# Performance work log

Measured on AMD Instinct MI355X. Metric: run time of the kernel, lower is better.

## Reference

```python
import jax, jax.numpy as jnp
import numpy as np

N = 100000          # total nodes
E = 1200000         # total edges
IN_CH = 22          # NUM_NODES_SINGLE_TEAM * 2
HID = 64
NUM_CLASSES = 3
G = 256             # graphs in batch


def setup_inputs() -> dict:
    key = jax.random.key(0)
    ks = jax.random.split(key, 12)
    x = jax.random.normal(ks[0], (N, IN_CH), jnp.float32)
    edge_index = jax.random.randint(ks[1], (2, E), 0, N, dtype=jnp.int32)
    edge_weight = jax.random.uniform(ks[2], (E,), jnp.float32)
    batch = jnp.sort(jax.random.randint(ks[3], (N,), 0, G, dtype=jnp.int32))

    def lin_w(k, fi, fo):
        return jax.random.normal(k, (fi, fo), jnp.float32) / np.float32(np.sqrt(fi))

    return {
        "x": x,
        "edge_index": edge_index,
        "edge_weight": edge_weight,
        "batch": batch,
        "W1": lin_w(ks[4], IN_CH, HID),  "b1": jnp.zeros((HID,), jnp.float32),
        "W2": lin_w(ks[5], HID, HID),    "b2": jnp.zeros((HID,), jnp.float32),
        "fw1": lin_w(ks[6], HID, HID),   "fb1": jnp.zeros((HID,), jnp.float32),
        "fw2": lin_w(ks[7], HID, NUM_CLASSES), "fb2": jnp.zeros((NUM_CLASSES,), jnp.float32),
    }


def gcn_conv(x, edge_index, edge_weight, W, b):
    """PyG GCNConv: self-loops (weight 1) + symmetric normalization + scatter-add."""
    n = x.shape[0]
    loop = jnp.arange(n, dtype=edge_index.dtype)
    row = jnp.concatenate([edge_index[0], loop])
    col = jnp.concatenate([edge_index[1], loop])
    w = jnp.concatenate([edge_weight, jnp.ones((n,), x.dtype)])
    deg = jax.ops.segment_sum(w, col, num_segments=n)        # weighted in-degree
    safe = jnp.where(deg > 0, deg, 1.0)
    dinv = jnp.where(deg > 0, jax.lax.rsqrt(safe), 0.0)
    norm = dinv[row] * w * dinv[col]                         # [E+N]
    h = x @ W                                                # transform first (d small)
    msg = norm[:, None] * h[row]                             # gather + scale
    out = jax.ops.segment_sum(msg, col, num_segments=n)      # scatter-add
    return out + b


def reference(x, edge_index, edge_weight, batch, W1, b1, W2, b2, fw1, fb1, fw2, fb2):
    h = jax.nn.relu(gcn_conv(x, edge_index, edge_weight, W1, b1))
    h = jax.nn.relu(gcn_conv(h, edge_index, edge_weight, W2, b2))
    # global_mean_pool
    sums = jax.ops.segment_sum(h, batch, num_segments=G)
    cnt = jax.ops.segment_sum(jnp.ones((h.shape[0],), h.dtype), batch, num_segments=G)
    pooled = sums / jnp.maximum(cnt, 1.0)[:, None]
    h = jax.nn.relu(pooled @ fw1 + fb1)
    return h @ fw2 + fb2
```

## Files before the change

### kernel.cpp

```cpp
#include <hip/hip_runtime.h>
#include <hip/hip_bf16.h>
#include <hip/hip_fp16.h>


#define HIDC 64
#define MTILE 128
#define XS_STRIDE (MTILE + 4)
#define BSHIFT 9
#define SPAN 512
#define NBKT_MAX 256
#define BCHUNK 2048

typedef unsigned long long u64;

__global__ void k_zero_int(int* p, int n) {
    int i = blockIdx.x * blockDim.x + threadIdx.x;
    if (i < n) p[i] = 0;
}

__global__ __launch_bounds__(256) void k_bin_count(const int* __restrict__ col,
                                                   int* bucket_cnt, int E, int NB) {
    __shared__ int hist[NBKT_MAX];
    int tid = threadIdx.x;
    for (int i = tid; i < NB; i += 256) hist[i] = 0;
    __syncthreads();
    int base = blockIdx.x * 8192;
    for (int j = 0; j < 32; ++j) {
        int e = base + j * 256 + tid;
        if (e < E) atomicAdd(&hist[col[e] >> BSHIFT], 1);
    }
    __syncthreads();
    for (int i = tid; i < NB; i += 256)
        if (hist[i]) atomicAdd(&bucket_cnt[i], hist[i]);
}

__global__ void k_bucket_scan(const int* __restrict__ bucket_cnt, int* __restrict__ bucket_base,
                              int* __restrict__ cursor_g, int NB, int E) {
    __shared__ int s[256];
    int t = threadIdx.x;
    int v = (t < NB) ? bucket_cnt[t] : 0;
    s[t] = v;
    __syncthreads();
    for (int o = 1; o < 256; o <<= 1) {
        int x = (t >= o) ? s[t - o] : 0;
        __syncthreads();
        s[t] += x;
        __syncthreads();
    }
    if (t < NB) { int ex = s[t] - v; bucket_base[t] = ex; cursor_g[t] = ex; }
    if (t == 0) bucket_base[NB] = E;
}

__global__ __launch_bounds__(256) void k_bin_scatter(const int* __restrict__ row,
                                                     const int* __restrict__ col,
                                                     const float* __restrict__ ew,
                                                     int* cursor_g, u64* __restrict__ bedges,
                                                     int E, int NB) {
    __shared__ int hist[NBKT_MAX], binoff[NBKT_MAX], cursor[NBKT_MAX], gbase[NBKT_MAX];
    __shared__ int s[256];
    __shared__ u64 stage[BCHUNK];
    __shared__ unsigned char binid[BCHUNK];
    int tid = threadIdx.x;
    for (int i = tid; i < NB; i += 256) hist[i] = 0;
    __syncthreads();
    int base = blockIdx.x * BCHUNK;
    u64 pk[8]; int bb[8];
#pragma unroll
    for (int j = 0; j < 8; ++j) {
        int e = base + j * 256 + tid;
        if (e < E) {
            int c = col[e];
            bb[j] = c >> BSHIFT;
            pk[j] = ((u64)__float_as_uint(ew[e]) << 32) |
                    ((u64)(unsigned)row[e] << BSHIFT) | (unsigned)(c & (SPAN - 1));
            atomicAdd(&hist[bb[j]], 1);
        } else bb[j] = -1;
    }
    __syncthreads();
    {
        int v = (tid < NB) ? hist[tid] : 0;
        s[tid] = v;
        __syncthreads();
        for (int o = 1; o < 256; o <<= 1) {
            int x = (tid >= o) ? s[tid - o] : 0;
            __syncthreads();
            s[tid] += x;
            __syncthreads();
        }
        if (tid < NB) { binoff[tid] = s[tid] - v; cursor[tid] = s[tid] - v; }
    }
    __syncthreads();
#pragma unroll
    for (int j = 0; j < 8; ++j)
        if (bb[j] >= 0) {
            int pos = atomicAdd(&cursor[bb[j]], 1);
            stage[pos] = pk[j];
            binid[pos] = (unsigned char)bb[j];
        }
    __syncthreads();
    if (tid < NB && hist[tid] > 0) gbase[tid] = atomicAdd(&cursor_g[tid], hist[tid]);
    __syncthreads();
    int total = min(BCHUNK, E - base);
    for (int i = tid; i < total; i += 256) {
        int b = binid[i];
        bedges[(size_t)gbase[b] + (i - binoff[b])] = stage[i];
    }
}

__global__ __launch_bounds__(256) void k_bucket_process(const u64* __restrict__ bedges,
                                                        const int* __restrict__ bucket_base,
                                                        u64* __restrict__ csr,
                                                        float* __restrict__ dinv,
                                                        int* __restrict__ off,
                                                        int N, int E, int NB) {
    __shared__ float deg[SPAN];
    __shared__ int cL[SPAN];
    __shared__ int offL[SPAN];
    __shared__ int s[256];
    int b = blockIdx.x, tid = threadIdx.x;
    int ebase = bucket_base[b], ecnt = bucket_base[b + 1] - ebase;
    int nd0 = b << BSHIFT;
    int ndn = min(SPAN, N - nd0);
    for (int i = tid; i < SPAN; i += 256) { deg[i] = 1.0f; cL[i] = 0; }
    __syncthreads();
    for (int e = tid; e < ecnt; e += 256) {
        u64 p = bedges[ebase + e];
        int colin = (int)(p & (SPAN - 1));
        atomicAdd(&deg[colin], __uint_as_float((unsigned)(p >> 32)));
        atomicAdd(&cL[colin], 1);
    }
    __syncthreads();
    int p0 = cL[2 * tid], p1 = cL[2 * tid + 1];
    s[tid] = p0 + p1;
    __syncthreads();
    for (int o = 1; o < 256; o <<= 1) {
        int x = (tid >= o) ? s[tid - o] : 0;
        __syncthreads();
        s[tid] += x;
        __syncthreads();
    }
    int ex = s[tid] - (p0 + p1);
    offL[2 * tid] = ex;
    offL[2 * tid + 1] = ex + p0;
    __syncthreads();
    for (int i = tid; i < ndn; i += 256) {
        dinv[nd0 + i] = rsqrtf(deg[i]);
        off[nd0 + i] = ebase + offL[i];
    }
    for (int i = tid; i < SPAN; i += 256) cL[i] = offL[i];
    if (b == NB - 1 && tid == 0) off[N] = E;
    __syncthreads();
    for (int e = tid; e < ecnt; e += 256) {
        u64 p = bedges[ebase + e];
        int colin = (int)(p & (SPAN - 1));
        int src = (int)((p >> BSHIFT) & 0x7FFFFF);
        int slot = atomicAdd(&cL[colin], 1);
        csr[(size_t)ebase + slot] = ((u64)(unsigned)src << 32) | (unsigned)(p >> 32);
    }
}

template <int K>
__global__ __launch_bounds__(256) void k_gemm_tile(const float* __restrict__ x,
                                                   const float* __restrict__ W,
                                                   const float* __restrict__ dinv,
                                                   __half* __restrict__ h, int n) {
    __shared__ float xs[K * XS_STRIDE];
    __shared__ float ws[K * HIDC];
    int tid = threadIdx.x;
    int n0 = blockIdx.x * MTILE;

    for (int i = tid; i < K * HIDC; i += 256) ws[i] = W[i];

    if constexpr ((K & 3) == 0) {
        constexpr int KQ = K / 4;
        for (int i = tid; i < MTILE * KQ; i += 256) {
            int r = i / KQ, kq = i - r * KQ;
            float4 v = make_float4(0.f, 0.f, 0.f, 0.f);
            if (n0 + r < n)
                v = *reinterpret_cast<const float4*>(x + (size_t)(n0 + r) * K + kq * 4);
            int k0 = kq * 4;
            xs[(k0 + 0) * XS_STRIDE + r] = v.x;
            xs[(k0 + 1) * XS_STRIDE + r] = v.y;
            xs[(k0 + 2) * XS_STRIDE + r] = v.z;
            xs[(k0 + 3) * XS_STRIDE + r] = v.w;
        }
    } else {
        for (int i = tid; i < MTILE * K; i += 256) {
            int r = i / K, k = i - r * K;
            float v = (n0 + r < n) ? x[(size_t)(n0 + r) * K + k] : 0.f;
            xs[k * XS_STRIDE + r] = v;
        }
    }
    __syncthreads();

    int c0 = (tid & 15) * 4;
    int m0 = (tid >> 4) * 8;
    float acc[8][4];
#pragma unroll
    for (int j = 0; j < 8; ++j)
#pragma unroll
        for (int q = 0; q < 4; ++q) acc[j][q] = 0.f;

#pragma unroll 4
    for (int k = 0; k < K; ++k) {
        float4 a0 = *reinterpret_cast<const float4*>(&xs[k * XS_STRIDE + m0]);
        float4 a1 = *reinterpret_cast<const float4*>(&xs[k * XS_STRIDE + m0 + 4]);
        float4 b  = *reinterpret_cast<const float4*>(&ws[k * HIDC + c0]);
        float av[8] = {a0.x, a0.y, a0.z, a0.w, a1.x, a1.y, a1.z, a1.w};
        float bv[4] = {b.x, b.y, b.z, b.w};
#pragma unroll
        for (int j = 0; j < 8; ++j)
#pragma unroll
            for (int q = 0; q < 4; ++q)
                acc[j][q] = fmaf(av[j], bv[q], acc[j][q]);
    }

#pragma unroll
    for (int j = 0; j < 8; ++j) {
        int node = n0 + m0 + j;
        if (node < n) {
            float dv = dinv[node];
            union { struct { __half2 a, b; } h2; float2 f2; } u;
            u.h2.a = __floats2half2_rn(acc[j][0] * dv, acc[j][1] * dv);
            u.h2.b = __floats2half2_rn(acc[j][2] * dv, acc[j][3] * dv);
            *reinterpret_cast<float2*>(h + (size_t)node * HIDC + c0) = u.f2;
        }
    }
}

__global__ void k_gcn_gather(const __half* __restrict__ h, const int* __restrict__ off,
                             const u64* __restrict__ csr, const float* __restrict__ dinv,
                             const float* __restrict__ bias, float* __restrict__ out, int n) {
    int t = blockIdx.x * blockDim.x + threadIdx.x;
    int lane = threadIdx.x & 63;
    int node = ((t >> 6) << 1) + (lane >> 5);
    int sub = lane & 31;
    if (node >= n) return;
    const __half2* hp = reinterpret_cast<const __half2*>(h);
    float d = dinv[node];
    float2 sv = __half22float2(hp[(size_t)node * 32 + sub]);
    float acc0 = sv.x, acc1 = sv.y;
    int i = off[node], e1 = off[node + 1];
    for (; i + 3 < e1; i += 4) {
        u64 eA = csr[i], eB = csr[i + 1], eC = csr[i + 2], eD = csr[i + 3];
        float2 hA = __half22float2(hp[(size_t)(eA >> 32) * 32 + sub]);
        float2 hB = __half22float2(hp[(size_t)(eB >> 32) * 32 + sub]);
        float2 hC = __half22float2(hp[(size_t)(eC >> 32) * 32 + sub]);
        float2 hD = __half22float2(hp[(size_t)(eD >> 32) * 32 + sub]);
        float wA = __uint_as_float((unsigned)eA);
        float wB = __uint_as_float((unsigned)eB);
        float wC = __uint_as_float((unsigned)eC);
        float wD = __uint_as_float((unsigned)eD);
        acc0 = fmaf(wA, hA.x, acc0); acc1 = fmaf(wA, hA.y, acc1);
        acc0 = fmaf(wB, hB.x, acc0); acc1 = fmaf(wB, hB.y, acc1);
        acc0 = fmaf(wC, hC.x, acc0); acc1 = fmaf(wC, hC.y, acc1);
        acc0 = fmaf(wD, hD.x, acc0); acc1 = fmaf(wD, hD.y, acc1);
    }
    for (; i < e1; ++i) {
        u64 eA = csr[i];
        float2 hA = __half22float2(hp[(size_t)(eA >> 32) * 32 + sub]);
        float wA = __uint_as_float((unsigned)eA);
        acc0 = fmaf(wA, hA.x, acc0); acc1 = fmaf(wA, hA.y, acc1);
    }
    int c0 = sub * 2;
    float2 o;
    o.x = fmaxf(fmaf(d, acc0, bias[c0]), 0.f);
    o.y = fmaxf(fmaf(d, acc1, bias[c0 + 1]), 0.f);
    *reinterpret_cast<float2*>(out + (size_t)node * HIDC + c0) = o;
}

__global__ void k_zero(float* p, int n) {
    int i = blockIdx.x * blockDim.x + threadIdx.x;
    if (i < n) p[i] = 0.f;
}

__global__ void k_pool(const float* __restrict__ h, const int* __restrict__ batch,
                       float* __restrict__ pooled, float* __restrict__ cnt, int n) {
    int c = threadIdx.x & 63, sub = threadIdx.x >> 6;
    int n0 = blockIdx.x * 256;
    int nend = min(n0 + 256, n);
    float acc = 0.f, cacc = 0.f;
    int curb = -1;
    for (int i = n0 + sub; i < nend; i += 4) {
        int b = batch[i];
        if (b != curb) {
            if (curb >= 0) {
                atomicAdd(&pooled[curb * HIDC + c], acc);
                if (c == 0) atomicAdd(&cnt[curb], cacc);
            }
            acc = 0.f; cacc = 0.f;
            curb = b;
        }
        acc += h[(size_t)i * HIDC + c];
        cacc += 1.f;
    }
    if (curb >= 0) {
        atomicAdd(&pooled[curb * HIDC + c], acc);
        if (c == 0) atomicAdd(&cnt[curb], cacc);
    }
}

__global__ void k_head(const float* __restrict__ pooled, const float* __restrict__ cnt,
                       const float* __restrict__ fw1, const float* __restrict__ fb1,
                       const float* __restrict__ fw2, const float* __restrict__ fb2,
                       float* __restrict__ out, int nclass) {
    int g = blockIdx.x;
    int j = threadIdx.x;
    __shared__ float p[HIDC], hid[HIDC];
    float c = fmaxf(cnt[g], 1.0f);
    p[j] = pooled[g * HIDC + j] / c;
    __syncthreads();
    float acc = fb1[j];
#pragma unroll 8
    for (int k = 0; k < HIDC; ++k) acc = fmaf(p[k], fw1[k * HIDC + j], acc);
    hid[j] = fmaxf(acc, 0.f);
    __syncthreads();
    if (j < nclass) {
        float o = fb2[j];
#pragma unroll 8
        for (int k = 0; k < HIDC; ++k) o = fmaf(hid[k], fw2[k * nclass + j], o);
        out[g * nclass + j] = o;
    }
}

extern "C" void kernel_launch(void* const* d_in, const int* in_sizes, int n_in,
                              void* d_out, int out_size, void* d_ws, size_t ws_size,
                              hipStream_t stream) {
    const float* x    = (const float*)d_in[0];
    const int* eidx   = (const int*)d_in[1];
    const float* ew   = (const float*)d_in[2];
    const int* batch  = (const int*)d_in[3];
    const float* W1   = (const float*)d_in[4];
    const float* b1   = (const float*)d_in[5];
    const float* W2   = (const float*)d_in[6];
    const float* b2   = (const float*)d_in[7];
    const float* fw1  = (const float*)d_in[8];
    const float* fb1  = (const float*)d_in[9];
    const float* fw2  = (const float*)d_in[10];
    const float* fb2  = (const float*)d_in[11];
    float* out = (float*)d_out;

    const int N = in_sizes[3];
    const int E = in_sizes[1] / 2;
    const int NCLASS = in_sizes[11];
    const int G = out_size / NCLASS;
    const int NB = (N + SPAN - 1) >> BSHIFT;

    const int* row = eidx;
    const int* col = eidx + E;

    char* wp = (char*)d_ws;
    u64*   bedges = (u64*)wp;    wp += sizeof(u64) * E;
    u64*   csr    = (u64*)wp;    wp += sizeof(u64) * E;
    float* dinv   = (float*)wp;  wp += sizeof(float) * N;
    __half* hbuf  = (__half*)wp; wp += sizeof(__half) * (size_t)N * HIDC;
    float* bufB   = (float*)wp;  wp += sizeof(float) * (size_t)N * HIDC;
    float* pooled = (float*)wp;  wp += sizeof(float) * (size_t)G * HIDC;
    float* cnt    = (float*)wp;  wp += sizeof(float) * G;
    int*   off    = (int*)wp;    wp += sizeof(int) * (N + 1);
    int*   bucket_cnt  = (int*)wp; wp += sizeof(int) * NBKT_MAX;
    int*   bucket_base = (int*)wp; wp += sizeof(int) * (NBKT_MAX + 1);
    int*   cursor_g    = (int*)wp; wp += sizeof(int) * NBKT_MAX;

    const int BLK = 256;
    dim3 blk(BLK);
    int gTile = (N + MTILE - 1) / MTILE;
    int gGather = (N + 7) / 8;

    k_zero_int<<<1, blk, 0, stream>>>(bucket_cnt, NB);
    k_bin_count<<<(E + 8191) / 8192, blk, 0, stream>>>(col, bucket_cnt, E, NB);
    k_bucket_scan<<<1, blk, 0, stream>>>(bucket_cnt, bucket_base, cursor_g, NB, E);
    k_bin_scatter<<<(E + BCHUNK - 1) / BCHUNK, blk, 0, stream>>>(row, col, ew, cursor_g,
                                                                 bedges, E, NB);
    k_bucket_process<<<NB, blk, 0, stream>>>(bedges, bucket_base, csr, dinv, off, N, E, NB);

    k_gemm_tile<22><<<gTile, blk, 0, stream>>>(x, W1, dinv, hbuf, N);
    k_gcn_gather<<<gGather, blk, 0, stream>>>(hbuf, off, csr, dinv, b1, bufB, N);

    k_gemm_tile<64><<<gTile, blk, 0, stream>>>(bufB, W2, dinv, hbuf, N);
    k_gcn_gather<<<gGather, blk, 0, stream>>>(hbuf, off, csr, dinv, b2, bufB, N);

    int zeroN = G * HIDC + G;
    k_zero<<<(zeroN + BLK - 1) / BLK, blk, 0, stream>>>(pooled, zeroN);
    k_pool<<<(N + 255) / 256, blk, 0, stream>>>(bufB, batch, pooled, cnt, N);

    k_head<<<G, dim3(64), 0, stream>>>(pooled, cnt, fw1, fb1, fw2, fb2, out, NCLASS);
}
```

Baseline: 215.7 us.

## Aggregate raw features before transform in first GCN layer, unroll gather by eight

The first layer now aggregates the 22-channel input, pre-scaled by dinv and stored as padded fp16, over the CSR. Only afterwards does it apply the 22x64 GEMM with fused bias and ReLU, so the gather moves 32 half channels per edge instead of 64. The cost is an extra prep kernel and an fp32 aggregate buffer, plus one more launch. The second-layer gather loop is unrolled to 8 edges with a 2-edge remainder to raise memory-level parallelism, and the k_gemm_tile load path is simplified to always use float4 since it is now only instantiated with K=64.

```diff
diff --git a/kernel.cpp b/kernel.cpp
--- a/kernel.cpp
+++ b/kernel.cpp
@@ -159,6 +159,114 @@
     }
 }
 
+__global__ void k_prep_x16(const float* __restrict__ x, const float* __restrict__ dinv,
+                           __half* __restrict__ x16, int n, int K) {
+    int t = blockIdx.x * blockDim.x + threadIdx.x;
+    int node = t >> 4, p = t & 15;
+    if (node >= n) return;
+    int c0 = p * 2;
+    float d = dinv[node];
+    float a = (c0 < K)     ? d * x[(size_t)node * K + c0]     : 0.f;
+    float b = (c0 + 1 < K) ? d * x[(size_t)node * K + c0 + 1] : 0.f;
+    reinterpret_cast<__half2*>(x16)[(size_t)node * 16 + p] = __floats2half2_rn(a, b);
+}
+
+__global__ void k_agg_x(const __half* __restrict__ x16, const int* __restrict__ off,
+                        const u64* __restrict__ csr, const float* __restrict__ dinv,
+                        float* __restrict__ agg, int n, int K) {
+    int t = blockIdx.x * blockDim.x + threadIdx.x;
+    int lane = threadIdx.x & 63;
+    int node = ((t >> 6) << 2) + (lane >> 4);
+    int sub = lane & 15;
+    if (node >= n) return;
+    const __half2* xp = reinterpret_cast<const __half2*>(x16);
+    float2 sv = __half22float2(xp[(size_t)node * 16 + sub]);
+    float acc0 = sv.x, acc1 = sv.y;
+    int i = off[node], e1 = off[node + 1];
+    for (; i + 3 < e1; i += 4) {
+        u64 eA = csr[i], eB = csr[i + 1], eC = csr[i + 2], eD = csr[i + 3];
+        float2 hA = __half22float2(xp[(size_t)(eA >> 32) * 16 + sub]);
+        float2 hB = __half22float2(xp[(size_t)(eB >> 32) * 16 + sub]);
+        float2 hC = __half22float2(xp[(size_t)(eC >> 32) * 16 + sub]);
+        float2 hD = __half22float2(xp[(size_t)(eD >> 32) * 16 + sub]);
+        float wA = __uint_as_float((unsigned)eA);
+        float wB = __uint_as_float((unsigned)eB);
+        float wC = __uint_as_float((unsigned)eC);
+        float wD = __uint_as_float((unsigned)eD);
+        acc0 = fmaf(wA, hA.x, acc0); acc1 = fmaf(wA, hA.y, acc1);
+        acc0 = fmaf(wB, hB.x, acc0); acc1 = fmaf(wB, hB.y, acc1);
+        acc0 = fmaf(wC, hC.x, acc0); acc1 = fmaf(wC, hC.y, acc1);
+        acc0 = fmaf(wD, hD.x, acc0); acc1 = fmaf(wD, hD.y, acc1);
+    }
+    for (; i < e1; ++i) {
+        u64 eA = csr[i];
+        float2 hA = __half22float2(xp[(size_t)(eA >> 32) * 16 + sub]);
+        float wA = __uint_as_float((unsigned)eA);
+        acc0 = fmaf(wA, hA.x, acc0); acc1 = fmaf(wA, hA.y, acc1);
+    }
+    int c0 = sub * 2;
+    if (c0 < K) {
+        float d = dinv[node];
+        float2 o; o.x = d * acc0; o.y = d * acc1;
+        *reinterpret_cast<float2*>(agg + (size_t)node * K + c0) = o;
+    }
+}
+
+template <int K>
+__global__ __launch_bounds__(256) void k_gemm_bias_relu(const float* __restrict__ x,
+                                                        const float* __restrict__ W,
+                                                        const float* __restrict__ bias,
+                                                        float* __restrict__ out, int n) {
+    __shared__ float xs[K * XS_STRIDE];
+    __shared__ float ws[K * HIDC];
+    int tid = threadIdx.x;
+    int n0 = blockIdx.x * MTILE;
+
+    for (int i = tid; i < K * HIDC; i += 256) ws[i] = W[i];
+    for (int i = tid; i < MTILE * K; i += 256) {
+        int r = i / K, k = i - r * K;
+        float v = (n0 + r < n) ? x[(size_t)(n0 + r) * K + k] : 0.f;
+        xs[k * XS_STRIDE + r] = v;
+    }
+    __syncthreads();
+
+    int c0 = (tid & 15) * 4;
+    int m0 = (tid >> 4) * 8;
+    float acc[8][4];
+#pragma unroll
+    for (int j = 0; j < 8; ++j)
+#pragma unroll
+        for (int q = 0; q < 4; ++q) acc[j][q] = 0.f;
+
+#pragma unroll 4
+    for (int k = 0; k < K; ++k) {
+        float4 a0 = *reinterpret_cast<const float4*>(&xs[k * XS_STRIDE + m0]);
+        float4 a1 = *reinterpret_cast<const float4*>(&xs[k * XS_STRIDE + m0 + 4]);
+        float4 b  = *reinterpret_cast<const float4*>(&ws[k * HIDC + c0]);
+        float av[8] = {a0.x, a0.y, a0.z, a0.w, a1.x, a1.y, a1.z, a1.w};
+        float bv[4] = {b.x, b.y, b.z, b.w};
+#pragma unroll
+        for (int j = 0; j < 8; ++j)
+#pragma unroll
+            for (int q = 0; q < 4; ++q)
+                acc[j][q] = fmaf(av[j], bv[q], acc[j][q]);
+    }
+
+    float4 bb = *reinterpret_cast<const float4*>(bias + c0);
+#pragma unroll
+    for (int j = 0; j < 8; ++j) {
+        int node = n0 + m0 + j;
+        if (node < n) {
+            float4 v;
+            v.x = fmaxf(acc[j][0] + bb.x, 0.f);
+            v.y = fmaxf(acc[j][1] + bb.y, 0.f);
+            v.z = fmaxf(acc[j][2] + bb.z, 0.f);
+            v.w = fmaxf(acc[j][3] + bb.w, 0.f);
+            *reinterpret_cast<float4*>(out + (size_t)node * HIDC + c0) = v;
+        }
+    }
+}
+
 template <int K>
 __global__ __launch_bounds__(256) void k_gemm_tile(const float* __restrict__ x,
                                                    const float* __restrict__ W,
@@ -171,25 +279,17 @@
 
     for (int i = tid; i < K * HIDC; i += 256) ws[i] = W[i];
 
-    if constexpr ((K & 3) == 0) {
-        constexpr int KQ = K / 4;
-        for (int i = tid; i < MTILE * KQ; i += 256) {
-            int r = i / KQ, kq = i - r * KQ;
-            float4 v = make_float4(0.f, 0.f, 0.f, 0.f);
-            if (n0 + r < n)
-                v = *reinterpret_cast<const float4*>(x + (size_t)(n0 + r) * K + kq * 4);
-            int k0 = kq * 4;
-            xs[(k0 + 0) * XS_STRIDE + r] = v.x;
-            xs[(k0 + 1) * XS_STRIDE + r] = v.y;
-            xs[(k0 + 2) * XS_STRIDE + r] = v.z;
-            xs[(k0 + 3) * XS_STRIDE + r] = v.w;
-        }
-    } else {
-        for (int i = tid; i < MTILE * K; i += 256) {
-            int r = i / K, k = i - r * K;
-            float v = (n0 + r < n) ? x[(size_t)(n0 + r) * K + k] : 0.f;
-            xs[k * XS_STRIDE + r] = v;
-        }
+    constexpr int KQ = K / 4;
+    for (int i = tid; i < MTILE * KQ; i += 256) {
+        int r = i / KQ, kq = i - r * KQ;
+        float4 v = make_float4(0.f, 0.f, 0.f, 0.f);
+        if (n0 + r < n)
+            v = *reinterpret_cast<const float4*>(x + (size_t)(n0 + r) * K + kq * 4);
+        int k0 = kq * 4;
+        xs[(k0 + 0) * XS_STRIDE + r] = v.x;
+        xs[(k0 + 1) * XS_STRIDE + r] = v.y;
+        xs[(k0 + 2) * XS_STRIDE + r] = v.z;
+        xs[(k0 + 3) * XS_STRIDE + r] = v.w;
     }
     __syncthreads();
 
@@ -241,22 +341,40 @@
     float2 sv = __half22float2(hp[(size_t)node * 32 + sub]);
     float acc0 = sv.x, acc1 = sv.y;
     int i = off[node], e1 = off[node + 1];
-    for (; i + 3 < e1; i += 4) {
-        u64 eA = csr[i], eB = csr[i + 1], eC = csr[i + 2], eD = csr[i + 3];
+    for (; i + 7 < e1; i += 8) {
+        u64 e0 = csr[i], e1_ = csr[i + 1], e2 = csr[i + 2], e3 = csr[i + 3];
+        u64 e4 = csr[i + 4], e5 = csr[i + 5], e6 = csr[i + 6], e7 = csr[i + 7];
+        float2 h0 = __half22float2(hp[(size_t)(e0 >> 32) * 32 + sub]);
+        float2 h1 = __half22float2(hp[(size_t)(e1_ >> 32) * 32 + sub]);
+        float2 h2 = __half22float2(hp[(size_t)(e2 >> 32) * 32 + sub]);
+        float2 h3 = __half22float2(hp[(size_t)(e3 >> 32) * 32 + sub]);
+        float2 h4 = __half22float2(hp[(size_t)(e4 >> 32) * 32 + sub]);
+        float2 h5 = __half22float2(hp[(size_t)(e5 >> 32) * 32 + sub]);
+        float2 h6 = __half22float2(hp[(size_t)(e6 >> 32) * 32 + sub]);
+        float2 h7 = __half22float2(hp[(size_t)(e7 >> 32) * 32 + sub]);
+        float w0 = __uint_as_float((unsigned)e0), w1 = __uint_as_float((unsigned)e1_);
+        float w2 = __uint_as_float((unsigned)e2), w3 = __uint_as_float((unsigned)e3);
+        float w4 = __uint_as_float((unsigned)e4), w5 = __uint_as_float((unsigned)e5);
+        float w6 = __uint_as_float((unsigned)e6), w7 = __uint_as_float((unsigned)e7);
+        acc0 = fmaf(w0, h0.x, acc0); acc1 = fmaf(w0, h0.y, acc1);
+        acc0 = fmaf(w1, h1.x, acc0); acc1 = fmaf(w1, h1.y, acc1);
+        acc0 = fmaf(w2, h2.x, acc0); acc1 = fmaf(w2, h2.y, acc1);
+        acc0 = fmaf(w3, h3.x, acc0); acc1 = fmaf(w3, h3.y, acc1);
+        acc0 = fmaf(w4, h4.x, acc0); acc1 = fmaf(w4, h4.y, acc1);
+        acc0 = fmaf(w5, h5.x, acc0); acc1 = fmaf(w5, h5.y, acc1);
+        acc0 = fmaf(w6, h6.x, acc0); acc1 = fmaf(w6, h6.y, acc1);
+        acc0 = fmaf(w7, h7.x, acc0); acc1 = fmaf(w7, h7.y, acc1);
+    }
+    for (; i + 1 < e1; i += 2) {
+        u64 eA = csr[i], eB = csr[i + 1];
         float2 hA = __half22float2(hp[(size_t)(eA >> 32) * 32 + sub]);
         float2 hB = __half22float2(hp[(size_t)(eB >> 32) * 32 + sub]);
-        float2 hC = __half22float2(hp[(size_t)(eC >> 32) * 32 + sub]);
-        float2 hD = __half22float2(hp[(size_t)(eD >> 32) * 32 + sub]);
         float wA = __uint_as_float((unsigned)eA);
         float wB = __uint_as_float((unsigned)eB);
-        float wC = __uint_as_float((unsigned)eC);
-        float wD = __uint_as_float((unsigned)eD);
         acc0 = fmaf(wA, hA.x, acc0); acc1 = fmaf(wA, hA.y, acc1);
         acc0 = fmaf(wB, hB.x, acc0); acc1 = fmaf(wB, hB.y, acc1);
-        acc0 = fmaf(wC, hC.x, acc0); acc1 = fmaf(wC, hC.y, acc1);
-        acc0 = fmaf(wD, hD.x, acc0); acc1 = fmaf(wD, hD.y, acc1);
-    }
-    for (; i < e1; ++i) {
+    }
+    if (i < e1) {
         u64 eA = csr[i];
         float2 hA = __half22float2(hp[(size_t)(eA >> 32) * 32 + sub]);
         float wA = __uint_as_float((unsigned)eA);
@@ -342,6 +460,7 @@
 
     const int N = in_sizes[3];
     const int E = in_sizes[1] / 2;
+    const int INCH = in_sizes[0] / N;
     const int NCLASS = in_sizes[11];
     const int G = out_size / NCLASS;
     const int NB = (N + SPAN - 1) >> BSHIFT;
@@ -353,6 +472,8 @@
     u64*   bedges = (u64*)wp;    wp += sizeof(u64) * E;
     u64*   csr    = (u64*)wp;    wp += sizeof(u64) * E;
     float* dinv   = (float*)wp;  wp += sizeof(float) * N;
+    __half* x16   = (__half*)wp; wp += sizeof(__half) * (size_t)N * 32;
+    float* agg    = (float*)wp;  wp += sizeof(float) * (size_t)N * INCH;
     __half* hbuf  = (__half*)wp; wp += sizeof(__half) * (size_t)N * HIDC;
     float* bufB   = (float*)wp;  wp += sizeof(float) * (size_t)N * HIDC;
     float* pooled = (float*)wp;  wp += sizeof(float) * (size_t)G * HIDC;
@@ -366,6 +487,8 @@
     dim3 blk(BLK);
     int gTile = (N + MTILE - 1) / MTILE;
     int gGather = (N + 7) / 8;
+    int gAggX   = (N + 15) / 16;
+    int gPrep   = ((size_t)N * 16 + BLK - 1) / BLK;
 
     k_zero_int<<<1, blk, 0, stream>>>(bucket_cnt, NB);
     k_bin_count<<<(E + 8191) / 8192, blk, 0, stream>>>(col, bucket_cnt, E, NB);
@@ -374,8 +497,9 @@
                                                                  bedges, E, NB);
     k_bucket_process<<<NB, blk, 0, stream>>>(bedges, bucket_base, csr, dinv, off, N, E, NB);
 
-    k_gemm_tile<22><<<gTile, blk, 0, stream>>>(x, W1, dinv, hbuf, N);
-    k_gcn_gather<<<gGather, blk, 0, stream>>>(hbuf, off, csr, dinv, b1, bufB, N);
+    k_prep_x16<<<gPrep, blk, 0, stream>>>(x, dinv, x16, N, INCH);
+    k_agg_x<<<gAggX, blk, 0, stream>>>(x16, off, csr, dinv, agg, N, INCH);
+    k_gemm_bias_relu<22><<<gTile, blk, 0, stream>>>(agg, W1, b1, bufB, N);
 
     k_gemm_tile<64><<<gTile, blk, 0, stream>>>(bufB, W2, dinv, hbuf, N);
     k_gcn_gather<<<gGather, blk, 0, stream>>>(hbuf, off, csr, dinv, b2, bufB, N);
```

Result: faster. 203.1 us (-5.8%).
